# Kernel optimization log

Measured on AMD Instinct MI355X. Metric: run time of the kernel, lower is better.

Reference implementation:

```python
import jax, jax.numpy as jnp
import numpy as np

B, S, HN, TN = 8, 32, 64, 512
HID, EMB, VOCAB = 512, 512, 10000


def setup_inputs():
    key = jax.random.key(0)
    k = jax.random.split(key, 14)
    w = lambda kk, shape: jax.random.normal(kk, shape, jnp.float32) * 0.02
    return {
        "dec_out": jax.random.normal(k[0], (B, S, HID), jnp.float32),
        "history": jax.random.normal(k[1], (B, HID), jnp.float32),
        "head": jax.random.randint(k[2], (B, HN), 0, VOCAB),
        "tail": jax.random.randint(k[3], (B, TN), 0, VOCAB),
        "adj_mask": jax.random.randint(k[4], (B, HN, TN), 0, 2).astype(bool),
        "dup_mask": jax.random.randint(k[5], (B, S, TN), 0, 2).astype(bool),
        "emb_table": w(k[6], (VOCAB, EMB)),
        "W_tq": w(k[7], (2 * HID + EMB, HID)),
        "b_tq": jnp.zeros((HID,), jnp.float32),
        "W_tk": w(k[8], (EMB, HID)),
        "b_tk": jnp.zeros((HID,), jnp.float32),
        "W_tout": w(k[9], (2 * HID, HID)),
        "W_hq": w(k[10], (2 * HID, HID)),
        "b_hq": jnp.zeros((HID,), jnp.float32),
        "W_hk": w(k[11], (HID, HID)),
        "b_hk": jnp.zeros((HID,), jnp.float32),
    }


def reference(dec_out, history, head, tail, adj_mask, dup_mask, emb_table,
              W_tq, b_tq, W_tk, b_tk, W_tout, W_hq, b_hq, W_hk, b_hk):
    head_emb = emb_table[head]  # (B, HN, EMB)
    tail_emb = emb_table[tail]  # (B, TN, EMB)

    # --- tail attention query: Linear(cat([dec_out, history, head_emb])) + ELU.
    # Same math as the torch broadcast-concat, computed as a sum of three
    # partial matmuls to avoid materializing the (B,S,HN,2*hid+emb) concat.
    Wd, Wh, We = W_tq[:HID], W_tq[HID:2 * HID], W_tq[2 * HID:]
    tq = jax.nn.elu((dec_out @ Wd)[:, :, None, :]
                    + (history @ Wh)[:, None, None, :]
                    + (head_emb @ We)[:, None, :, :]
                    + b_tq)                       # (B, S, HN, HID)
    tq = tq.reshape(B, S * HN, HID)
    tk = jax.nn.elu(tail_emb @ W_tk + b_tk)       # (B, TN, HID)  (dropout=eval)

    # combined logical mask: allowed = adjacency AND not-duplicate
    mask = (adj_mask[:, None, :, :] & ~dup_mask[:, :, None, :]).reshape(B, S * HN, TN)

    # GlobalAttention (dot): score -> mask -> softmax -> context -> tanh(linear_out([c;q]))
    scores = jnp.einsum('bqh,bth->bqt', tq, tk)   # (B, S*HN, TN)
    tail_attn = jax.nn.softmax(jnp.where(mask, scores, -jnp.inf), axis=-1)
    ctx = jnp.einsum('bqt,bth->bqh', tail_attn, tk)
    graph_hid = jnp.tanh(ctx @ W_tout[:HID] + tq @ W_tout[HID:])
    graph_hid = graph_hid.reshape(B * S, HN, HID)
    tail_attn = tail_attn.reshape(B * S, HN, TN)

    # --- head attention (one-step), length-masked over HN
    hq = jax.nn.elu(dec_out @ W_hq[:HID] + (history @ W_hq[HID:])[:, None, :] + b_hq)
    hq = hq.reshape(B * S, HID)
    hk = jax.nn.elu(jnp.einsum('nkh,hd->nkd', graph_hid, W_hk) + b_hk)
    lengths = jnp.repeat(jnp.sum(head != 0, axis=-1), S)          # (B*S,)
    hscores = jnp.einsum('nh,nkh->nk', hq, hk)                    # (B*S, HN)
    lmask = jnp.arange(HN)[None, :] < lengths[:, None]
    head_attn = jax.nn.softmax(jnp.where(lmask, hscores, -jnp.inf), axis=-1)
    # (head-attention context output is discarded by the original module)

    prob = jnp.einsum('nk,nkt->nt', head_attn, tail_attn).reshape(B, S, TN)
    return jnp.log(prob + 1e-20)
```

## Files before the change

kernel.cpp:

```cpp
#include <hip/hip_runtime.h>
#include <math.h>

#define BB 8
#define SS 32
#define HN 64
#define TN 512
#define HID 512

typedef __attribute__((ext_vector_type(8))) short short8;
typedef __attribute__((ext_vector_type(4))) float f32x4;

__device__ __forceinline__ float eluf(float x) { return x > 0.f ? x : (expf(x) - 1.f); }

__device__ __forceinline__ short f2bs(float f) {
    union { float f; unsigned int u; } v; v.f = f;
    unsigned int r = v.u + 0x7fffu + ((v.u >> 16) & 1u);
    return (short)(r >> 16);
}
__device__ __forceinline__ float b2f(short s) {
    union { unsigned int u; float f; } v;
    v.u = ((unsigned int)(unsigned short)s) << 16;
    return v.f;
}

__device__ __forceinline__ void gld16(const void* g, void* l) {
    __builtin_amdgcn_global_load_lds(
        (const __attribute__((address_space(1))) void*)g,
        (__attribute__((address_space(3))) void*)l, 16, 0, 0);
}

template <int ACT, int OUTB, int DUAL>
__device__ __forceinline__ void gcore(
    const short* __restrict__ A, const short* __restrict__ B,
    const short* __restrict__ A2, const short* __restrict__ B2,
    const float* __restrict__ bias, void* __restrict__ Cv,
    int ldc, int K, int m0, int n0, int cm0, short* Ls)
{
    short* Al = Ls;
    short* Bl = Ls + 4096;
    const int tid  = threadIdx.x;
    const int lane = tid & 63;
    const int w    = tid >> 6;
    const int wr   = w >> 1, wc = w & 1;
    const int l16  = lane & 15, quad = lane >> 4;

    const int srow = w * 16 + (lane >> 2);
    const int scol = (lane & 3) * 8;

    f32x4 acc[4][4];
#pragma unroll
    for (int i = 0; i < 4; ++i)
#pragma unroll
        for (int j = 0; j < 4; ++j) { acc[i][j][0]=0.f; acc[i][j][1]=0.f; acc[i][j][2]=0.f; acc[i][j][3]=0.f; }

    short* lA = Al + w * 512;
    short* lB = Bl + w * 512;
    const long rstep = (long)64 * K;

    for (int rep = 0; rep <= DUAL; ++rep) {
        const short* Ag = (rep ? A2 : A) + (long)(m0 + srow) * K + scol;
        const short* Bg = (rep ? B2 : B) + (long)(n0 + srow) * K + scol;
        for (int kt = 0; kt < K; kt += 32) {
            __syncthreads();
            gld16(Ag + kt, lA);
            gld16(Ag + kt + rstep, lA + 2048);
            gld16(Bg + kt, lB);
            gld16(Bg + kt + rstep, lB + 2048);
            __syncthreads();
            short8 af[4], bf4[4];
#pragma unroll
            for (int mi = 0; mi < 4; ++mi)
                af[mi] = *(const short8*)(Al + (wr * 64 + mi * 16 + l16) * 32 + quad * 8);
#pragma unroll
            for (int ni = 0; ni < 4; ++ni)
                bf4[ni] = *(const short8*)(Bl + (wc * 64 + ni * 16 + l16) * 32 + quad * 8);
#pragma unroll
            for (int mi = 0; mi < 4; ++mi)
#pragma unroll
                for (int ni = 0; ni < 4; ++ni)
                    acc[mi][ni] = __builtin_amdgcn_mfma_f32_16x16x32_bf16(af[mi], bf4[ni], acc[mi][ni], 0, 0, 0);
        }
    }

    __syncthreads();

    float bv[4];
#pragma unroll
    for (int ni = 0; ni < 4; ++ni)
        bv[ni] = bias ? bias[n0 + wc * 64 + ni * 16 + l16] : 0.f;

    if (OUTB) {
        short* eb = Ls + w * 1152;
        const int er = lane >> 2;
        const int ec = (lane & 3) * 16;
#pragma unroll
        for (int mi = 0; mi < 4; ++mi) {
#pragma unroll
            for (int ni = 0; ni < 4; ++ni)
#pragma unroll
                for (int r = 0; r < 4; ++r) {
                    float x = acc[mi][ni][r] + bv[ni];
                    if (ACT == 1) x = eluf(x);
                    else if (ACT == 2) x = tanhf(x);
                    eb[(quad * 4 + r) * 72 + ni * 16 + l16] = f2bs(x);
                }
            __builtin_amdgcn_sched_barrier(0);
            short8 v0 = *(const short8*)&eb[er * 72 + ec];
            short8 v1 = *(const short8*)&eb[er * 72 + ec + 8];
            long cb = (long)(cm0 + wr * 64 + mi * 16 + er) * ldc + n0 + wc * 64 + ec;
            *(short8*)((short*)Cv + cb)     = v0;
            *(short8*)((short*)Cv + cb + 8) = v1;
            __builtin_amdgcn_sched_barrier(0);
        }
    } else {
#pragma unroll
        for (int mi = 0; mi < 4; ++mi)
#pragma unroll
            for (int ni = 0; ni < 4; ++ni) {
                int gc = n0 + wc * 64 + ni * 16 + l16;
#pragma unroll
                for (int r = 0; r < 4; ++r) {
                    float x = acc[mi][ni][r] + bv[ni];
                    if (ACT == 1) x = eluf(x);
                    else if (ACT == 2) x = tanhf(x);
                    ((float*)Cv)[(long)(cm0 + wr * 64 + mi * 16 + quad * 4 + r) * ldc + gc] = x;
                }
            }
    }
}

template <int ACT, int OUTB, int DUAL>
__global__ __launch_bounds__(256) void mgemm(
    const short* __restrict__ A, long sAz,
    const short* __restrict__ B, long sBz,
    const short* __restrict__ A2, long sA2z,
    const short* __restrict__ B2,
    const float* __restrict__ bias,
    void* __restrict__ Cv, long sCz, int ldc, int K)
{
    __shared__ short Ls[8192];
    const int z = blockIdx.z;
    void* C = OUTB ? (void*)((short*)Cv + (long)z * sCz) : (void*)((float*)Cv + (long)z * sCz);
    const short* A2z = DUAL ? (A2 + (long)z * sA2z) : nullptr;
    gcore<ACT, OUTB, DUAL>(A + (long)z * sAz, B + (long)z * sBz, A2z, B2, bias, C,
                           ldc, K, blockIdx.y * 128, blockIdx.x * 128, blockIdx.y * 128, Ls);
}

__global__ __launch_bounds__(256) void mgemm_multi(
    const short* __restrict__ decb, const short* __restrict__ WTall, float* __restrict__ qall,
    const short* __restrict__ embAll, const short* __restrict__ WTe, float* __restrict__ qe,
    const short* __restrict__ WTk, const float* __restrict__ b_tk, short* __restrict__ tkb)
{
    __shared__ short Ls[8192];
    int id = blockIdx.x;
    if (id < 48) {
        int y = id >> 4, x = id & 15;
        gcore<0, 0, 0>(decb, WTall, nullptr, nullptr, nullptr, qall, 2048, 512,
                       y * 128, x * 128, y * 128, Ls);
    } else if (id < 64) {
        int id2 = id - 48, y = id2 >> 2, x = id2 & 3;
        gcore<0, 0, 0>(embAll, WTe, nullptr, nullptr, nullptr, qe, 512, 512,
                       y * 128, x * 128, y * 128, Ls);
    } else {
        int id3 = id - 64, y = id3 >> 2, x = id3 & 3;
        gcore<1, 1, 0>(embAll, WTk, nullptr, nullptr, b_tk, tkb, 512, 512,
                       512 + y * 128, x * 128, y * 128, Ls);
    }
}

struct WTDesc { const float* src[9]; short* dst[9]; };

__global__ __launch_bounds__(256) void prep(
    const float* __restrict__ dec_out, const float* __restrict__ history,
    short* __restrict__ decb,
    const float* __restrict__ emb, const int* __restrict__ head, const int* __restrict__ tail,
    short* __restrict__ embAll, WTDesc wd)
{
    __shared__ float t[32][33];
    const int id = blockIdx.x, tid = threadIdx.x;
    if (id < 528) {
        int i = id * 256 + tid;
        float v = (i < 131072) ? dec_out[i] : history[i - 131072];
        decb[i] = f2bs(v);
    } else if (id < 528 + 4608) {
        int r = id - 528;
        int idx = (r < 512) ? head[r] : tail[r - 512];
        const float* s = emb + (long)idx * 512;
        short* dst = embAll + (long)r * 512;
        dst[tid]       = f2bs(s[tid]);
        dst[tid + 256] = f2bs(s[tid + 256]);
    } else {
        int q = id - 5136;
        int z = q >> 8, xy = q & 255;
        int x = xy & 15, y = xy >> 4;
        const float* src = wd.src[z];
        short* dst = wd.dst[z];
        int k0 = y * 32, n0 = x * 32;
        int tx = tid & 31, ty = tid >> 5;
#pragma unroll
        for (int i = 0; i < 32; i += 8)
            t[ty + i][tx] = src[(long)(k0 + ty + i) * 512 + n0 + tx];
        __syncthreads();
#pragma unroll
        for (int i = 0; i < 32; i += 8)
            dst[(long)(n0 + ty + i) * 512 + k0 + tx] = f2bs(t[tx][ty + i]);
    }
}

__global__ __launch_bounds__(256) void l3_kernel(
    const float* __restrict__ qall, const float* __restrict__ qe,
    const float* __restrict__ b_tq, short* __restrict__ tqb,
    const short* __restrict__ WTo1, const short* __restrict__ tkb, short* __restrict__ tkWTb)
{
    __shared__ short Ls[8192];
    if (blockIdx.x < 8192) {
        long gid = (long)blockIdx.x * 256 + threadIdx.x;
        int r = (int)(gid >> 7), j0 = ((int)gid & 127) * 4;
        int b = r >> 11, rem = r & 2047, s = rem >> 6, h = rem & 63;
        float4 d = *(const float4*)(qall + (long)(b * 32 + s) * 2048 + j0);
        float4 q = *(const float4*)(qall + (long)(256 + b) * 2048 + 1024 + j0);
        float4 e = *(const float4*)(qe + (long)(b * 64 + h) * 512 + j0);
        float4 bb = *(const float4*)(b_tq + j0);
        short4 o;
        o.x = f2bs(eluf(d.x + q.x + e.x + bb.x));
        o.y = f2bs(eluf(d.y + q.y + e.y + bb.y));
        o.z = f2bs(eluf(d.z + q.z + e.z + bb.z));
        o.w = f2bs(eluf(d.w + q.w + e.w + bb.w));
        *(short4*)(tqb + (long)r * 512 + j0) = o;
    } else {
        int id2 = blockIdx.x - 8192;
        int z = id2 >> 4, r = id2 & 15;
        int x = r & 3, y = r >> 2;
        gcore<0, 1, 0>(WTo1, tkb + (long)z * 262144, nullptr, nullptr, nullptr,
                       tkWTb + (long)z * 262144, 512, 512, y * 128, x * 128, y * 128, Ls);
    }
}

__global__ __launch_bounds__(256) void sm_kernel(
    const short* __restrict__ sc, const int* __restrict__ adj, const int* __restrict__ dup,
    short* __restrict__ Pb)
{
    int w = threadIdx.x >> 6, lane = threadIdx.x & 63;
    long r = (long)blockIdx.x * 4 + w;
    int b = (int)(r >> 11), rem = (int)(r & 2047), s = rem >> 6, h = rem & 63;
    const short* row = sc + r * 512 + lane * 8;
    const int* adjr = adj + ((long)(b * 64 + h)) * 512 + lane * 8;
    const int* dupr = dup + ((long)(b * 32 + s)) * 512 + lane * 8;
    short8 v8 = *(const short8*)row;
    int4 a0 = *(const int4*)adjr, a1 = *(const int4*)(adjr + 4);
    int4 d0 = *(const int4*)dupr, d1 = *(const int4*)(dupr + 4);
    int am[8] = {a0.x, a0.y, a0.z, a0.w, a1.x, a1.y, a1.z, a1.w};
    int dm[8] = {d0.x, d0.y, d0.z, d0.w, d1.x, d1.y, d1.z, d1.w};
    float v[8];
    float m = -INFINITY;
#pragma unroll
    for (int i = 0; i < 8; ++i) {
        v[i] = (am[i] && !dm[i]) ? b2f(v8[i]) : -INFINITY;
        m = fmaxf(m, v[i]);
    }
#pragma unroll
    for (int d = 32; d >= 1; d >>= 1) m = fmaxf(m, __shfl_xor(m, d));
    float sum = 0.f;
#pragma unroll
    for (int i = 0; i < 8; ++i) {
        float e = (m == -INFINITY) ? 0.f : expf(v[i] - m);
        v[i] = e; sum += e;
    }
#pragma unroll
    for (int d = 32; d >= 1; d >>= 1) sum += __shfl_xor(sum, d);
    float inv = sum > 0.f ? 1.f / sum : 0.f;
    short8 o;
#pragma unroll
    for (int i = 0; i < 8; ++i) o[i] = f2bs(v[i] * inv);
    *(short8*)(Pb + r * 512 + lane * 8) = o;
}

__global__ __launch_bounds__(256) void fused_head(
    const float* __restrict__ qall, const float* __restrict__ b_hq,
    const short* __restrict__ hk, const int* __restrict__ head,
    const short* __restrict__ ta, float* __restrict__ out)
{
    int n = blockIdx.x, b = n >> 5;
    int tid = threadIdx.x;
    __shared__ float hql[512];
    __shared__ float hsl[64];
    __shared__ float hal[64];
    __shared__ float part[4][512];

    for (int j = tid; j < 512; j += 256)
        hql[j] = eluf(qall[(long)n * 2048 + 512 + j] + qall[(long)(256 + b) * 2048 + 1536 + j] + b_hq[j]);
    __syncthreads();

    {
        int k = tid >> 2, p = tid & 3;
        const short* hkr = hk + ((long)n * 64 + k) * 512 + p * 128;
        const float* hq0 = hql + p * 128;
        float a = 0.f;
#pragma unroll 4
        for (int jj = 0; jj < 128; jj += 8) {
            short8 hv = *(const short8*)(hkr + jj);
#pragma unroll
            for (int u = 0; u < 8; ++u) a += b2f(hv[u]) * hq0[jj + u];
        }
        a += __shfl_xor(a, 1);
        a += __shfl_xor(a, 2);
        if (p == 0) hsl[k] = a;
    }
    __syncthreads();

    if (tid < 64) {
        int hv = head[b * 64 + tid];
        unsigned long long ball = __ballot(hv != 0);
        int len = __popcll(ball);
        float sv = (tid < len) ? hsl[tid] : -INFINITY;
        float m = sv;
#pragma unroll
        for (int d = 32; d >= 1; d >>= 1) m = fmaxf(m, __shfl_xor(m, d));
        float e = expf(sv - m);
        float sum = e;
#pragma unroll
        for (int d = 32; d >= 1; d >>= 1) sum += __shfl_xor(sum, d);
        hal[tid] = e / sum;
    }
    __syncthreads();

    {
        int w = tid >> 6, lane = tid & 63;
        const short* tab = ta + (long)n * 64 * 512 + (long)(w * 16) * 512 + lane * 8;
        float acc[8] = {};
#pragma unroll
        for (int k = 0; k < 16; ++k) {
            float a = hal[w * 16 + k];
            short8 tv = *(const short8*)(tab + (long)k * 512);
#pragma unroll
            for (int u = 0; u < 8; ++u) acc[u] += a * b2f(tv[u]);
        }
        float4* pp = (float4*)&part[w][lane * 8];
        pp[0] = make_float4(acc[0], acc[1], acc[2], acc[3]);
        pp[1] = make_float4(acc[4], acc[5], acc[6], acc[7]);
    }
    __syncthreads();

    for (int t = tid; t < 512; t += 256) {
        float a = part[0][t] + part[1][t] + part[2][t] + part[3][t];
        out[(long)n * 512 + t] = logf(a + 1e-20f);
    }
}

extern "C" void kernel_launch(void* const* d_in, const int* in_sizes, int n_in,
                              void* d_out, int out_size, void* d_ws, size_t ws_size,
                              hipStream_t stream)
{
    const float* dec_out = (const float*)d_in[0];
    const float* history = (const float*)d_in[1];
    const int*   head    = (const int*)d_in[2];
    const int*   tail    = (const int*)d_in[3];
    const int*   adj     = (const int*)d_in[4];
    const int*   dup     = (const int*)d_in[5];
    const float* emb     = (const float*)d_in[6];
    const float* W_tq    = (const float*)d_in[7];
    const float* b_tq    = (const float*)d_in[8];
    const float* W_tk    = (const float*)d_in[9];
    const float* b_tk    = (const float*)d_in[10];
    const float* W_tout  = (const float*)d_in[11];
    const float* W_hq    = (const float*)d_in[12];
    const float* b_hq    = (const float*)d_in[13];
    const float* W_hk    = (const float*)d_in[14];
    const float* b_hk    = (const float*)d_in[15];
    float* out = (float*)d_out;

    char* ws = (char*)d_ws;
    auto alloc = [&](size_t bytes) -> void* {
        char* p = ws;
        ws += (bytes + 255) & ~(size_t)255;
        return (void*)p;
    };
    short* decb   = (short*)alloc((size_t)384 * 512 * 2);
    short* embAll = (short*)alloc((size_t)4608 * 512 * 2);
    short* WT     = (short*)alloc((size_t)9 * 512 * 512 * 2);
    float* qall   = (float*)alloc((size_t)384 * 2048 * 4);
    float* qe     = (float*)alloc((size_t)512 * 512 * 4);
    short* tkb    = (short*)alloc((size_t)4096 * 512 * 2);
    short* tkWTb  = (short*)alloc((size_t)4096 * 512 * 2);
    short* tqb    = (short*)alloc((size_t)16384 * 512 * 2);
    short* scb    = (short*)alloc((size_t)16384 * 512 * 2);
    short* Pb     = (short*)alloc((size_t)16384 * 512 * 2);
    short* ghb = scb;
    short* hkb = tqb;

    WTDesc wd;
    wd.src[0] = W_tq;               wd.dst[0] = WT;
    wd.src[1] = W_hq;               wd.dst[1] = WT + (size_t)1 * 262144;
    wd.src[2] = W_tq + 512 * 512;   wd.dst[2] = WT + (size_t)2 * 262144;
    wd.src[3] = W_hq + 512 * 512;   wd.dst[3] = WT + (size_t)3 * 262144;
    wd.src[4] = W_tq + 1024 * 512;  wd.dst[4] = WT + (size_t)4 * 262144;
    wd.src[5] = W_tk;               wd.dst[5] = WT + (size_t)5 * 262144;
    wd.src[6] = W_tout;             wd.dst[6] = WT + (size_t)6 * 262144;
    wd.src[7] = W_tout + 512 * 512; wd.dst[7] = WT + (size_t)7 * 262144;
    wd.src[8] = W_hk;               wd.dst[8] = WT + (size_t)8 * 262144;

    prep<<<7440, 256, 0, stream>>>(dec_out, history, decb, emb, head, tail, embAll, wd);
    mgemm_multi<<<192, 256, 0, stream>>>(decb, WT, qall, embAll, WT + (size_t)4 * 262144, qe,
                                         WT + (size_t)5 * 262144, b_tk, tkb);
    l3_kernel<<<8320, 256, 0, stream>>>(qall, qe, b_tq, tqb, WT + (size_t)6 * 262144, tkb, tkWTb);
    mgemm<0, 1, 0><<<dim3(4, 16, 8), 256, 0, stream>>>(
        tqb, (long)2048 * 512, tkb, 262144, nullptr, 0, nullptr, nullptr,
        scb, (long)2048 * 512, 512, 512);
    sm_kernel<<<4096, 256, 0, stream>>>(scb, adj, dup, Pb);
    mgemm<2, 1, 1><<<dim3(4, 16, 8), 256, 0, stream>>>(
        Pb, (long)2048 * 512, tkWTb, 262144, tqb, (long)2048 * 512, WT + (size_t)7 * 262144,
        nullptr, ghb, (long)2048 * 512, 512, 512);
    mgemm<1, 1, 0><<<dim3(4, 128, 1), 256, 0, stream>>>(
        ghb, 0, WT + (size_t)8 * 262144, 0, nullptr, 0, nullptr, b_hk,
        hkb, 0, 512, 512);
    fused_head<<<256, 256, 0, stream>>>(qall, b_hq, hkb, head, Pb, out);
}
```

Measured before the change: 237.1 us.

## Fuse head-score dot product into hk GEMM epilogue and double GEMM K-step

The hk GEMM epilogue now applies ELU and dots each row with the precomputed head query. It writes per-column-tile partial head scores instead of storing the full bf16 hk matrix, and fused_head just sums the four partials. The head query ELU is computed in extra blocks of l3_kernel. Separately, every GEMM now loads 64-wide K slices per barrier pair, with LDS doubled to 32KB, which halves the syncs but may lower occupancy.

```diff
diff --git a/kernel.cpp b/kernel.cpp
--- a/kernel.cpp
+++ b/kernel.cpp
@@ -34,10 +34,11 @@
     const short* __restrict__ A, const short* __restrict__ B,
     const short* __restrict__ A2, const short* __restrict__ B2,
     const float* __restrict__ bias, void* __restrict__ Cv,
-    int ldc, int K, int m0, int n0, int cm0, short* Ls)
+    int ldc, int K, int m0, int n0, int cm0, short* Ls,
+    const float* __restrict__ hq, float* __restrict__ hsp)
 {
     short* Al = Ls;
-    short* Bl = Ls + 4096;
+    short* Bl = Ls + 8192;
     const int tid  = threadIdx.x;
     const int lane = tid & 63;
     const int w    = tid >> 6;
@@ -60,25 +61,32 @@
     for (int rep = 0; rep <= DUAL; ++rep) {
         const short* Ag = (rep ? A2 : A) + (long)(m0 + srow) * K + scol;
         const short* Bg = (rep ? B2 : B) + (long)(n0 + srow) * K + scol;
-        for (int kt = 0; kt < K; kt += 32) {
+        for (int kt = 0; kt < K; kt += 64) {
             __syncthreads();
             gld16(Ag + kt, lA);
             gld16(Ag + kt + rstep, lA + 2048);
+            gld16(Ag + kt + 32, lA + 4096);
+            gld16(Ag + kt + 32 + rstep, lA + 4096 + 2048);
             gld16(Bg + kt, lB);
             gld16(Bg + kt + rstep, lB + 2048);
+            gld16(Bg + kt + 32, lB + 4096);
+            gld16(Bg + kt + 32 + rstep, lB + 4096 + 2048);
             __syncthreads();
-            short8 af[4], bf4[4];
-#pragma unroll
-            for (int mi = 0; mi < 4; ++mi)
-                af[mi] = *(const short8*)(Al + (wr * 64 + mi * 16 + l16) * 32 + quad * 8);
-#pragma unroll
-            for (int ni = 0; ni < 4; ++ni)
-                bf4[ni] = *(const short8*)(Bl + (wc * 64 + ni * 16 + l16) * 32 + quad * 8);
-#pragma unroll
-            for (int mi = 0; mi < 4; ++mi)
+#pragma unroll
+            for (int h = 0; h < 2; ++h) {
+                short8 af[4], bf4[4];
+#pragma unroll
+                for (int mi = 0; mi < 4; ++mi)
+                    af[mi] = *(const short8*)(Al + h * 4096 + (wr * 64 + mi * 16 + l16) * 32 + quad * 8);
 #pragma unroll
                 for (int ni = 0; ni < 4; ++ni)
-                    acc[mi][ni] = __builtin_amdgcn_mfma_f32_16x16x32_bf16(af[mi], bf4[ni], acc[mi][ni], 0, 0, 0);
+                    bf4[ni] = *(const short8*)(Bl + h * 4096 + (wc * 64 + ni * 16 + l16) * 32 + quad * 8);
+#pragma unroll
+                for (int mi = 0; mi < 4; ++mi)
+#pragma unroll
+                    for (int ni = 0; ni < 4; ++ni)
+                        acc[mi][ni] = __builtin_amdgcn_mfma_f32_16x16x32_bf16(af[mi], bf4[ni], acc[mi][ni], 0, 0, 0);
+            }
         }
     }
 
@@ -89,7 +97,7 @@
     for (int ni = 0; ni < 4; ++ni)
         bv[ni] = bias ? bias[n0 + wc * 64 + ni * 16 + l16] : 0.f;
 
-    if (OUTB) {
+    if (OUTB == 1) {
         short* eb = Ls + w * 1152;
         const int er = lane >> 2;
         const int ec = (lane & 3) * 16;
@@ -112,6 +120,36 @@
             *(short8*)((short*)Cv + cb + 8) = v1;
             __builtin_amdgcn_sched_barrier(0);
         }
+    } else if (OUTB == 2) {
+        const int n_w = (cm0 + wr * 64) >> 6;
+        float hqv[4];
+#pragma unroll
+        for (int ni = 0; ni < 4; ++ni)
+            hqv[ni] = hq[(long)n_w * 512 + n0 + wc * 64 + ni * 16 + l16];
+        float* red = (float*)Ls;
+#pragma unroll
+        for (int mi = 0; mi < 4; ++mi)
+#pragma unroll
+            for (int r = 0; r < 4; ++r) {
+                float p = 0.f;
+#pragma unroll
+                for (int ni = 0; ni < 4; ++ni) {
+                    float x = acc[mi][ni][r] + bv[ni];
+                    if (ACT == 1) x = eluf(x);
+                    p += x * hqv[ni];
+                }
+                p += __shfl_xor(p, 1);
+                p += __shfl_xor(p, 2);
+                p += __shfl_xor(p, 4);
+                p += __shfl_xor(p, 8);
+                if (l16 == 0) red[w * 64 + mi * 16 + quad * 4 + r] = p;
+            }
+        __syncthreads();
+        if (tid < 128) {
+            int wr2 = tid >> 6, rw = tid & 63;
+            float v = red[(wr2 * 2 + 0) * 64 + rw] + red[(wr2 * 2 + 1) * 64 + rw];
+            hsp[(long)(n0 >> 7) * 16384 + cm0 + tid] = v;
+        }
     } else {
 #pragma unroll
         for (int mi = 0; mi < 4; ++mi)
@@ -138,12 +176,22 @@
     const float* __restrict__ bias,
     void* __restrict__ Cv, long sCz, int ldc, int K)
 {
-    __shared__ short Ls[8192];
+    __shared__ short Ls[16384];
     const int z = blockIdx.z;
     void* C = OUTB ? (void*)((short*)Cv + (long)z * sCz) : (void*)((float*)Cv + (long)z * sCz);
     const short* A2z = DUAL ? (A2 + (long)z * sA2z) : nullptr;
     gcore<ACT, OUTB, DUAL>(A + (long)z * sAz, B + (long)z * sBz, A2z, B2, bias, C,
-                           ldc, K, blockIdx.y * 128, blockIdx.x * 128, blockIdx.y * 128, Ls);
+                           ldc, K, blockIdx.y * 128, blockIdx.x * 128, blockIdx.y * 128, Ls,
+                           nullptr, nullptr);
+}
+
+__global__ __launch_bounds__(256) void mgemm_hs(
+    const short* __restrict__ A, const short* __restrict__ B,
+    const float* __restrict__ bias, const float* __restrict__ hq, float* __restrict__ hsp)
+{
+    __shared__ short Ls[16384];
+    gcore<1, 2, 0>(A, B, nullptr, nullptr, bias, nullptr, 512, 512,
+                   blockIdx.y * 128, blockIdx.x * 128, blockIdx.y * 128, Ls, hq, hsp);
 }
 
 __global__ __launch_bounds__(256) void mgemm_multi(
@@ -151,20 +199,20 @@
     const short* __restrict__ embAll, const short* __restrict__ WTe, float* __restrict__ qe,
     const short* __restrict__ WTk, const float* __restrict__ b_tk, short* __restrict__ tkb)
 {
-    __shared__ short Ls[8192];
+    __shared__ short Ls[16384];
     int id = blockIdx.x;
     if (id < 48) {
         int y = id >> 4, x = id & 15;
         gcore<0, 0, 0>(decb, WTall, nullptr, nullptr, nullptr, qall, 2048, 512,
-                       y * 128, x * 128, y * 128, Ls);
+                       y * 128, x * 128, y * 128, Ls, nullptr, nullptr);
     } else if (id < 64) {
         int id2 = id - 48, y = id2 >> 2, x = id2 & 3;
         gcore<0, 0, 0>(embAll, WTe, nullptr, nullptr, nullptr, qe, 512, 512,
-                       y * 128, x * 128, y * 128, Ls);
+                       y * 128, x * 128, y * 128, Ls, nullptr, nullptr);
     } else {
         int id3 = id - 64, y = id3 >> 2, x = id3 & 3;
         gcore<1, 1, 0>(embAll, WTk, nullptr, nullptr, b_tk, tkb, 512, 512,
-                       512 + y * 128, x * 128, y * 128, Ls);
+                       512 + y * 128, x * 128, y * 128, Ls, nullptr, nullptr);
     }
 }
 
@@ -210,9 +258,10 @@
 __global__ __launch_bounds__(256) void l3_kernel(
     const float* __restrict__ qall, const float* __restrict__ qe,
     const float* __restrict__ b_tq, short* __restrict__ tqb,
-    const short* __restrict__ WTo1, const short* __restrict__ tkb, short* __restrict__ tkWTb)
-{
-    __shared__ short Ls[8192];
+    const short* __restrict__ WTo1, const short* __restrict__ tkb, short* __restrict__ tkWTb,
+    const float* __restrict__ b_hq, float* __restrict__ hqf)
+{
+    __shared__ short Ls[16384];
     if (blockIdx.x < 8192) {
         long gid = (long)blockIdx.x * 256 + threadIdx.x;
         int r = (int)(gid >> 7), j0 = ((int)gid & 127) * 4;
@@ -227,12 +276,26 @@
         o.z = f2bs(eluf(d.z + q.z + e.z + bb.z));
         o.w = f2bs(eluf(d.w + q.w + e.w + bb.w));
         *(short4*)(tqb + (long)r * 512 + j0) = o;
-    } else {
+    } else if (blockIdx.x < 8320) {
         int id2 = blockIdx.x - 8192;
         int z = id2 >> 4, r = id2 & 15;
         int x = r & 3, y = r >> 2;
         gcore<0, 1, 0>(WTo1, tkb + (long)z * 262144, nullptr, nullptr, nullptr,
-                       tkWTb + (long)z * 262144, 512, 512, y * 128, x * 128, y * 128, Ls);
+                       tkWTb + (long)z * 262144, 512, 512, y * 128, x * 128, y * 128, Ls,
+                       nullptr, nullptr);
+    } else {
+        long gid = (long)(blockIdx.x - 8320) * 256 + threadIdx.x;
+        int n = (int)(gid >> 7), j0 = ((int)gid & 127) * 4;
+        int b = n >> 5;
+        float4 d = *(const float4*)(qall + (long)n * 2048 + 512 + j0);
+        float4 h2 = *(const float4*)(qall + (long)(256 + b) * 2048 + 1536 + j0);
+        float4 bb = *(const float4*)(b_hq + j0);
+        float4 o;
+        o.x = eluf(d.x + h2.x + bb.x);
+        o.y = eluf(d.y + h2.y + bb.y);
+        o.z = eluf(d.z + h2.z + bb.z);
+        o.w = eluf(d.w + h2.w + bb.w);
+        *(float4*)(hqf + (long)n * 512 + j0) = o;
     }
 }
 
@@ -276,43 +339,21 @@
 }
 
 __global__ __launch_bounds__(256) void fused_head(
-    const float* __restrict__ qall, const float* __restrict__ b_hq,
-    const short* __restrict__ hk, const int* __restrict__ head,
+    const float* __restrict__ hsp, const int* __restrict__ head,
     const short* __restrict__ ta, float* __restrict__ out)
 {
     int n = blockIdx.x, b = n >> 5;
     int tid = threadIdx.x;
-    __shared__ float hql[512];
-    __shared__ float hsl[64];
     __shared__ float hal[64];
     __shared__ float part[4][512];
 
-    for (int j = tid; j < 512; j += 256)
-        hql[j] = eluf(qall[(long)n * 2048 + 512 + j] + qall[(long)(256 + b) * 2048 + 1536 + j] + b_hq[j]);
-    __syncthreads();
-
-    {
-        int k = tid >> 2, p = tid & 3;
-        const short* hkr = hk + ((long)n * 64 + k) * 512 + p * 128;
-        const float* hq0 = hql + p * 128;
-        float a = 0.f;
-#pragma unroll 4
-        for (int jj = 0; jj < 128; jj += 8) {
-            short8 hv = *(const short8*)(hkr + jj);
-#pragma unroll
-            for (int u = 0; u < 8; ++u) a += b2f(hv[u]) * hq0[jj + u];
-        }
-        a += __shfl_xor(a, 1);
-        a += __shfl_xor(a, 2);
-        if (p == 0) hsl[k] = a;
-    }
-    __syncthreads();
-
     if (tid < 64) {
+        float sv_raw = hsp[n * 64 + tid] + hsp[16384 + n * 64 + tid]
+                     + hsp[2 * 16384 + n * 64 + tid] + hsp[3 * 16384 + n * 64 + tid];
         int hv = head[b * 64 + tid];
         unsigned long long ball = __ballot(hv != 0);
         int len = __popcll(ball);
-        float sv = (tid < len) ? hsl[tid] : -INFINITY;
+        float sv = (tid < len) ? sv_raw : -INFINITY;
         float m = sv;
 #pragma unroll
         for (int d = 32; d >= 1; d >>= 1) m = fmaxf(m, __shfl_xor(m, d));
@@ -380,13 +421,14 @@
     short* WT     = (short*)alloc((size_t)9 * 512 * 512 * 2);
     float* qall   = (float*)alloc((size_t)384 * 2048 * 4);
     float* qe     = (float*)alloc((size_t)512 * 512 * 4);
+    float* hqf    = (float*)alloc((size_t)256 * 512 * 4);
+    float* hsp    = (float*)alloc((size_t)4 * 16384 * 4);
     short* tkb    = (short*)alloc((size_t)4096 * 512 * 2);
     short* tkWTb  = (short*)alloc((size_t)4096 * 512 * 2);
     short* tqb    = (short*)alloc((size_t)16384 * 512 * 2);
     short* scb    = (short*)alloc((size_t)16384 * 512 * 2);
     short* Pb     = (short*)alloc((size_t)16384 * 512 * 2);
     short* ghb = scb;
-    short* hkb = tqb;
 
     WTDesc wd;
     wd.src[0] = W_tq;               wd.dst[0] = WT;
@@ -402,7 +444,8 @@
     prep<<<7440, 256, 0, stream>>>(dec_out, history, decb, emb, head, tail, embAll, wd);
     mgemm_multi<<<192, 256, 0, stream>>>(decb, WT, qall, embAll, WT + (size_t)4 * 262144, qe,
                                          WT + (size_t)5 * 262144, b_tk, tkb);
-    l3_kernel<<<8320, 256, 0, stream>>>(qall, qe, b_tq, tqb, WT + (size_t)6 * 262144, tkb, tkWTb);
+    l3_kernel<<<8448, 256, 0, stream>>>(qall, qe, b_tq, tqb, WT + (size_t)6 * 262144, tkb, tkWTb,
+                                        b_hq, hqf);
     mgemm<0, 1, 0><<<dim3(4, 16, 8), 256, 0, stream>>>(
         tqb, (long)2048 * 512, tkb, 262144, nullptr, 0, nullptr, nullptr,
         scb, (long)2048 * 512, 512, 512);
@@ -410,8 +453,6 @@
     mgemm<2, 1, 1><<<dim3(4, 16, 8), 256, 0, stream>>>(
         Pb, (long)2048 * 512, tkWTb, 262144, tqb, (long)2048 * 512, WT + (size_t)7 * 262144,
         nullptr, ghb, (long)2048 * 512, 512, 512);
-    mgemm<1, 1, 0><<<dim3(4, 128, 1), 256, 0, stream>>>(
-        ghb, 0, WT + (size_t)8 * 262144, 0, nullptr, 0, nullptr, b_hk,
-        hkb, 0, 512, 512);
-    fused_head<<<256, 256, 0, stream>>>(qall, b_hq, hkb, head, Pb, out);
-}
+    mgemm_hs<<<dim3(4, 128), 256, 0, stream>>>(ghb, WT + (size_t)8 * 262144, b_hk, hqf, hsp);
+    fused_head<<<256, 256, 0, stream>>>(hsp, head, Pb, out);
+}
```

New measurement: 224.4 us. 5.4% less time.
